# Kernel optimization log

Hardware: AMD Instinct MI355X
Metric: run time of the kernel (lower is better)

Reference implementation:

```python
import jax, jax.numpy as jnp
import numpy as np

N_QUBITS = 8
NUM_HEADS = 2
EPS = 1e-5
TWO_PI = 6.283185307179586


def _rx(state, wire, theta, n):
    # state: (B, 2**n) complex64; theta: (B,) float. PennyLane wire 0 = MSB.
    B = state.shape[0]
    st = state.reshape(B, 2 ** wire, 2, 2 ** (n - 1 - wire))
    c = jnp.cos(theta * 0.5).astype(state.dtype)[:, None, None]
    s = ((-1j) * jnp.sin(theta * 0.5).astype(state.dtype))[:, None, None]
    a0 = st[:, :, 0, :]
    a1 = st[:, :, 1, :]
    return jnp.stack([c * a0 + s * a1, s * a0 + c * a1], axis=2).reshape(B, -1)


def _cnot(state, ctrl, tgt, n):
    B = state.shape[0]
    st = state.reshape((B,) + (2,) * n)
    ax_c = ctrl + 1
    ax_t = tgt + 1
    s0 = jnp.take(st, 0, axis=ax_c)
    s1 = jnp.take(st, 1, axis=ax_c)
    ft = ax_t - 1 if ax_t > ax_c else ax_t
    s1 = jnp.flip(s1, axis=ft)
    return jnp.stack([s0, s1], axis=ax_c).reshape(B, -1)


def _vqc(x, weights):
    # AngleEmbedding (RX) + BasicEntanglerLayers (RX per wire + CNOT ring) -> <Z_i>.
    # x: (B, n) angles; weights: (L, n). Returns (B, n) real expvals.
    B, n = x.shape
    state = jnp.zeros((B, 2 ** n), dtype=jnp.complex64).at[:, 0].set(1.0)
    for w in range(n):
        state = _rx(state, w, x[:, w], n)
    pairs = [(i, (i + 1) % n) for i in range(n)] if n > 2 else ([(0, 1)] if n == 2 else [])
    for l in range(weights.shape[0]):
        for w in range(n):
            state = _rx(state, w, jnp.broadcast_to(weights[l, w], (B,)), n)
        for cw, tw in pairs:
            state = _cnot(state, cw, tw, n)
    probs = (state.real ** 2 + state.imag ** 2).reshape((B,) + (2,) * n)
    zs = []
    for w in range(n):
        axes = tuple(a for a in range(1, n + 1) if a != w + 1)
        p = jnp.sum(probs, axis=axes)  # (B, 2)
        zs.append(p[:, 0] - p[:, 1])
    return jnp.stack(zs, axis=-1)


def _layernorm(x, g, b):
    m = jnp.mean(x, axis=-1, keepdims=True)
    v = jnp.mean((x - m) ** 2, axis=-1, keepdims=True)
    return (x - m) / jnp.sqrt(v + EPS) * g + b


def setup_inputs() -> dict:
    key = jax.random.key(0)
    ks = jax.random.split(key, 10)
    E = N_QUBITS
    x = jax.random.normal(ks[0], (64, 256, E), dtype=jnp.float32)
    # TorchLayer default init: uniform(0, 2*pi)
    Wq = jax.random.uniform(ks[1], (1, E), dtype=jnp.float32) * TWO_PI
    Wk = jax.random.uniform(ks[2], (1, E), dtype=jnp.float32) * TWO_PI
    Wv = jax.random.uniform(ks[3], (1, E), dtype=jnp.float32) * TWO_PI
    Wc = jax.random.uniform(ks[4], (1, E), dtype=jnp.float32) * TWO_PI
    Wf = jax.random.uniform(ks[5], (1, E), dtype=jnp.float32) * TWO_PI
    w1 = jax.random.normal(ks[6], (E, E), dtype=jnp.float32) * 0.3
    b1 = jax.random.normal(ks[7], (E,), dtype=jnp.float32) * 0.05
    w2 = jax.random.normal(ks[8], (E, E), dtype=jnp.float32) * 0.3
    b2 = jax.random.normal(ks[9], (E,), dtype=jnp.float32) * 0.05
    gamma1 = jnp.ones((E,), dtype=jnp.float32)
    beta1 = jnp.zeros((E,), dtype=jnp.float32)
    gamma2 = jnp.ones((E,), dtype=jnp.float32)
    beta2 = jnp.zeros((E,), dtype=jnp.float32)
    return {"x": x, "Wq": Wq, "Wk": Wk, "Wv": Wv, "Wc": Wc, "Wf": Wf,
            "w1": w1, "b1": b1, "w2": w2, "b2": b2,
            "gamma1": gamma1, "beta1": beta1, "gamma2": gamma2, "beta2": beta2}


def reference(x, Wq, Wk, Wv, Wc, Wf, w1, b1, w2, b2, gamma1, beta1, gamma2, beta2):
    B, S, E = x.shape
    H = NUM_HEADS
    dk = E // H
    tok = x.reshape(B * S, E)
    Q = _vqc(tok, Wq).reshape(B, S, E)
    K = _vqc(tok, Wk).reshape(B, S, E)
    V = _vqc(tok, Wv).reshape(B, S, E)
    split = lambda t: t.reshape(B, S, H, dk).transpose(0, 2, 1, 3)
    scores = jnp.einsum('bhqd,bhkd->bhqk', split(Q), split(K)) / jnp.sqrt(jnp.float32(dk))
    attn = jax.nn.softmax(scores, axis=-1)  # dropout = identity in eval
    ctx = jnp.einsum('bhqk,bhkd->bhqd', attn, split(V)).transpose(0, 2, 1, 3).reshape(B, S, E)
    attn_out = _vqc(ctx.reshape(B * S, E), Wc).reshape(B, S, E)
    x = _layernorm(x + attn_out, gamma1, beta1)
    h = x @ w1.T + b1                       # linear1 (no activation in FeedForwardQuantum)
    hq = _vqc(h.reshape(B * S, -1), Wf).reshape(B, S, -1)
    ff = hq @ w2.T + b2                     # linear2
    x = _layernorm(x + ff, gamma2, beta2)
    return x
```

## Files before the change

kernel.cpp:

```cpp
#include <hip/hip_runtime.h>


#define SEQ 256
#define EMB 8
#define QG  64
#define NSPLIT 4

static __device__ __forceinline__ void load8f(const float* __restrict__ p, float v[8]) {
    float4 a = *reinterpret_cast<const float4*>(p);
    float4 b = *reinterpret_cast<const float4*>(p + 4);
    v[0] = a.x; v[1] = a.y; v[2] = a.z; v[3] = a.w;
    v[4] = b.x; v[5] = b.y; v[6] = b.z; v[7] = b.w;
}

static __device__ __forceinline__ void store8f(float* __restrict__ p, const float v[8]) {
    *reinterpret_cast<float4*>(p)     = make_float4(v[0], v[1], v[2], v[3]);
    *reinterpret_cast<float4*>(p + 4) = make_float4(v[4], v[5], v[6], v[7]);
}

static __device__ __forceinline__ void vqc8(const float in[8], const float W[8], float z[8]) {
    float c[8];
#pragma unroll
    for (int i = 0; i < 8; ++i) c[i] = __cosf(in[i] + W[i]);
    float t = c[1];
#pragma unroll
    for (int i = 2; i < 8; ++i) t *= c[i];
    z[0] = t;
    float acc = c[0];
#pragma unroll
    for (int i = 1; i < 8; ++i) { acc *= c[i]; z[i] = acc; }
}

static __device__ __forceinline__ void ln8(const float r[8], const float g[8], const float be[8], float o[8]) {
    float m = 0.f;
#pragma unroll
    for (int i = 0; i < 8; ++i) m += r[i];
    m *= 0.125f;
    float var = 0.f;
#pragma unroll
    for (int i = 0; i < 8; ++i) { float d = r[i] - m; var += d * d; }
    var *= 0.125f;
    float inv = rsqrtf(var + 1e-5f);
#pragma unroll
    for (int i = 0; i < 8; ++i) o[i] = (r[i] - m) * inv * g[i] + be[i];
}

__global__ __launch_bounds__(512) void vitq_kernel(
    const float* __restrict__ x,
    const float* __restrict__ Wq, const float* __restrict__ Wk,
    const float* __restrict__ Wv, const float* __restrict__ Wc,
    const float* __restrict__ Wf,
    const float* __restrict__ w1, const float* __restrict__ b1,
    const float* __restrict__ w2, const float* __restrict__ b2,
    const float* __restrict__ g1, const float* __restrict__ be1,
    const float* __restrict__ g2, const float* __restrict__ be2,
    float* __restrict__ out)
{
    __shared__ float Ks[SEQ][EMB];
    __shared__ float Vs[SEQ][EMB];
    __shared__ float P[NSPLIT][2 * QG][5];

    const int bi  = blockIdx.x;
    const int b   = bi >> 2;
    const int g   = bi & 3;
    const int tid = threadIdx.x;
    const int p   = tid & 127;
    const int j   = tid >> 7;
    const int sl  = p & 63;
    const int h   = p >> 6;
    const int s   = g * QG + sl;

    const float* xb = x + ((size_t)b * SEQ) * EMB;

    float xq[8], wrow[8], q[8];
    load8f(xb + (size_t)s * EMB, xq);
    load8f(Wq, wrow);
    vqc8(xq, wrow, q);

    {
        const int t = tid & 255;
        float xs[8], kv[8];
        load8f(xb + (size_t)t * EMB, xs);
        if (tid < 256) {
            load8f(Wk, wrow);
            vqc8(xs, wrow, kv);
            store8f(&Ks[t][0], kv);
        } else {
            load8f(Wv, wrow);
            vqc8(xs, wrow, kv);
            store8f(&Vs[t][0], kv);
        }
    }
    __syncthreads();

    const int ho = 4 * h;
    float qh[4];
#pragma unroll
    for (int d = 0; d < 4; ++d) qh[d] = q[ho + d] * 0.5f;

    float l = 0.f, acc0 = 0.f, acc1 = 0.f, acc2 = 0.f, acc3 = 0.f;
    const int k0 = j * 64;
#pragma unroll 8
    for (int kk = k0; kk < k0 + 64; ++kk) {
        float4 kr = *reinterpret_cast<const float4*>(&Ks[kk][ho]);
        float4 vr = *reinterpret_cast<const float4*>(&Vs[kk][ho]);
        float sc = qh[0] * kr.x + qh[1] * kr.y + qh[2] * kr.z + qh[3] * kr.w;
        float e  = __expf(sc);
        l    += e;
        acc0 += e * vr.x;
        acc1 += e * vr.y;
        acc2 += e * vr.z;
        acc3 += e * vr.w;
    }
    P[j][p][0] = l;
    P[j][p][1] = acc0;
    P[j][p][2] = acc1;
    P[j][p][3] = acc2;
    P[j][p][4] = acc3;
    __syncthreads();

    if (tid < QG) {
        float ctx[8];
#pragma unroll
        for (int hh = 0; hh < 2; ++hh) {
            const int pp = hh * QG + tid;
            float ll = 0.f, a0 = 0.f, a1 = 0.f, a2 = 0.f, a3 = 0.f;
#pragma unroll
            for (int jj = 0; jj < NSPLIT; ++jj) {
                ll += P[jj][pp][0];
                a0 += P[jj][pp][1];
                a1 += P[jj][pp][2];
                a2 += P[jj][pp][3];
                a3 += P[jj][pp][4];
            }
            float inv = 1.f / ll;
            ctx[4 * hh + 0] = a0 * inv;
            ctx[4 * hh + 1] = a1 * inv;
            ctx[4 * hh + 2] = a2 * inv;
            ctx[4 * hh + 3] = a3 * inv;
        }

        float ao[8];
        load8f(Wc, wrow);
        vqc8(ctx, wrow, ao);

        float r[8];
#pragma unroll
        for (int i = 0; i < 8; ++i) r[i] = xq[i] + ao[i];

        float gg[8], be[8], x1[8];
        load8f(g1, gg); load8f(be1, be);
        ln8(r, gg, be, x1);

        float wf[64], bias[8];
#pragma unroll
        for (int i = 0; i < 64; ++i) wf[i] = w1[i];
        load8f(b1, bias);
        float hv[8];
#pragma unroll
        for (int jj = 0; jj < 8; ++jj) {
            float a = bias[jj];
#pragma unroll
            for (int i = 0; i < 8; ++i) a += x1[i] * wf[jj * 8 + i];
            hv[jj] = a;
        }

        float hq[8];
        load8f(Wf, wrow);
        vqc8(hv, wrow, hq);

#pragma unroll
        for (int i = 0; i < 64; ++i) wf[i] = w2[i];
        load8f(b2, bias);
        float r2[8];
#pragma unroll
        for (int jj = 0; jj < 8; ++jj) {
            float a = bias[jj];
#pragma unroll
            for (int i = 0; i < 8; ++i) a += hq[i] * wf[jj * 8 + i];
            r2[jj] = x1[jj] + a;
        }

        float o[8];
        load8f(g2, gg); load8f(be2, be);
        ln8(r2, gg, be, o);

        store8f(out + ((size_t)(b * SEQ + s)) * EMB, o);
    }
}

extern "C" void kernel_launch(void* const* d_in, const int* in_sizes, int n_in,
                              void* d_out, int out_size, void* d_ws, size_t ws_size,
                              hipStream_t stream) {
    const float* x   = (const float*)d_in[0];
    const float* Wq  = (const float*)d_in[1];
    const float* Wk  = (const float*)d_in[2];
    const float* Wv  = (const float*)d_in[3];
    const float* Wc  = (const float*)d_in[4];
    const float* Wf  = (const float*)d_in[5];
    const float* w1  = (const float*)d_in[6];
    const float* b1  = (const float*)d_in[7];
    const float* w2  = (const float*)d_in[8];
    const float* b2  = (const float*)d_in[9];
    const float* g1  = (const float*)d_in[10];
    const float* be1 = (const float*)d_in[11];
    const float* g2  = (const float*)d_in[12];
    const float* be2 = (const float*)d_in[13];
    float* out = (float*)d_out;

    const int B = in_sizes[0] / (SEQ * EMB);
    vitq_kernel<<<B * 4, 512, 0, stream>>>(x, Wq, Wk, Wv, Wc, Wf, w1, b1, w2, b2,
                                           g1, be1, g2, be2, out);
}
```

Measured before the change: 86.93 us.

## Register-block four queries per thread and split keys sixteen ways

Each thread now computes Q for four query rows of one head and walks a 16-key slice, so every K/V row read from shared memory is reused across four queries instead of one. The key dimension is split across 16 thread groups, which means more partial results to reduce in shared memory at the end, and the per-thread register footprint grows. The query input row is reloaded later for the residual.

```diff
diff --git a/kernel.cpp b/kernel.cpp
--- a/kernel.cpp
+++ b/kernel.cpp
@@ -4,7 +4,8 @@
 #define SEQ 256
 #define EMB 8
 #define QG  64
-#define NSPLIT 4
+#define NSPLIT 16
+#define KS  16
 
 static __device__ __forceinline__ void load8f(const float* __restrict__ p, float v[8]) {
     float4 a = *reinterpret_cast<const float4*>(p);
@@ -56,26 +57,20 @@
     const float* __restrict__ g2, const float* __restrict__ be2,
     float* __restrict__ out)
 {
-    __shared__ float Ks[SEQ][EMB];
-    __shared__ float Vs[SEQ][EMB];
-    __shared__ float P[NSPLIT][2 * QG][5];
+    __shared__ float K2[SEQ][2][4];
+    __shared__ float V2[SEQ][2][4];
+    __shared__ float P[NSPLIT][2][QG][5];
 
     const int bi  = blockIdx.x;
     const int b   = bi >> 2;
     const int g   = bi & 3;
     const int tid = threadIdx.x;
-    const int p   = tid & 127;
-    const int j   = tid >> 7;
-    const int sl  = p & 63;
-    const int h   = p >> 6;
-    const int s   = g * QG + sl;
+    const int qq  = tid & 15;
+    const int h   = (tid >> 4) & 1;
+    const int j   = tid >> 5;
 
     const float* xb = x + ((size_t)b * SEQ) * EMB;
-
-    float xq[8], wrow[8], q[8];
-    load8f(xb + (size_t)s * EMB, xq);
-    load8f(Wq, wrow);
-    vqc8(xq, wrow, q);
+    float wrow[8];
 
     {
         const int t = tid & 255;
@@ -84,61 +79,75 @@
         if (tid < 256) {
             load8f(Wk, wrow);
             vqc8(xs, wrow, kv);
-            store8f(&Ks[t][0], kv);
+            store8f(&K2[t][0][0], kv);
         } else {
             load8f(Wv, wrow);
             vqc8(xs, wrow, kv);
-            store8f(&Vs[t][0], kv);
-        }
+            store8f(&V2[t][0][0], kv);
+        }
+    }
+
+    float qh[4][4];
+    load8f(Wq, wrow);
+#pragma unroll
+    for (int m = 0; m < 4; ++m) {
+        const int s = g * QG + 4 * qq + m;
+        float xq[8], q[8];
+        load8f(xb + (size_t)s * EMB, xq);
+        vqc8(xq, wrow, q);
+#pragma unroll
+        for (int d = 0; d < 4; ++d) qh[m][d] = q[4 * h + d] * 0.5f;
     }
     __syncthreads();
 
-    const int ho = 4 * h;
-    float qh[4];
-#pragma unroll
-    for (int d = 0; d < 4; ++d) qh[d] = q[ho + d] * 0.5f;
-
-    float l = 0.f, acc0 = 0.f, acc1 = 0.f, acc2 = 0.f, acc3 = 0.f;
-    const int k0 = j * 64;
-#pragma unroll 8
-    for (int kk = k0; kk < k0 + 64; ++kk) {
-        float4 kr = *reinterpret_cast<const float4*>(&Ks[kk][ho]);
-        float4 vr = *reinterpret_cast<const float4*>(&Vs[kk][ho]);
-        float sc = qh[0] * kr.x + qh[1] * kr.y + qh[2] * kr.z + qh[3] * kr.w;
-        float e  = __expf(sc);
-        l    += e;
-        acc0 += e * vr.x;
-        acc1 += e * vr.y;
-        acc2 += e * vr.z;
-        acc3 += e * vr.w;
-    }
-    P[j][p][0] = l;
-    P[j][p][1] = acc0;
-    P[j][p][2] = acc1;
-    P[j][p][3] = acc2;
-    P[j][p][4] = acc3;
+    float l[4] = {0.f, 0.f, 0.f, 0.f};
+    float a0[4] = {0.f, 0.f, 0.f, 0.f};
+    float a1[4] = {0.f, 0.f, 0.f, 0.f};
+    float a2[4] = {0.f, 0.f, 0.f, 0.f};
+    float a3[4] = {0.f, 0.f, 0.f, 0.f};
+#pragma unroll 4
+    for (int i = 0; i < KS; ++i) {
+        const int kk = j * KS + i;
+        float4 kr = *reinterpret_cast<const float4*>(&K2[kk][h][0]);
+        float4 vr = *reinterpret_cast<const float4*>(&V2[kk][h][0]);
+#pragma unroll
+        for (int m = 0; m < 4; ++m) {
+            float sc = qh[m][0] * kr.x + qh[m][1] * kr.y + qh[m][2] * kr.z + qh[m][3] * kr.w;
+            float e  = __expf(sc);
+            l[m]  += e;
+            a0[m] += e * vr.x;
+            a1[m] += e * vr.y;
+            a2[m] += e * vr.z;
+            a3[m] += e * vr.w;
+        }
+    }
+#pragma unroll
+    for (int m = 0; m < 4; ++m) {
+        float* pp = &P[j][h][4 * qq + m][0];
+        pp[0] = l[m]; pp[1] = a0[m]; pp[2] = a1[m]; pp[3] = a2[m]; pp[4] = a3[m];
+    }
     __syncthreads();
 
     if (tid < QG) {
+        const int s = g * QG + tid;
         float ctx[8];
 #pragma unroll
         for (int hh = 0; hh < 2; ++hh) {
-            const int pp = hh * QG + tid;
-            float ll = 0.f, a0 = 0.f, a1 = 0.f, a2 = 0.f, a3 = 0.f;
+            float ll = 0.f, c0 = 0.f, c1 = 0.f, c2 = 0.f, c3 = 0.f;
 #pragma unroll
             for (int jj = 0; jj < NSPLIT; ++jj) {
-                ll += P[jj][pp][0];
-                a0 += P[jj][pp][1];
-                a1 += P[jj][pp][2];
-                a2 += P[jj][pp][3];
-                a3 += P[jj][pp][4];
+                const float* pp = &P[jj][hh][tid][0];
+                ll += pp[0]; c0 += pp[1]; c1 += pp[2]; c2 += pp[3]; c3 += pp[4];
             }
             float inv = 1.f / ll;
-            ctx[4 * hh + 0] = a0 * inv;
-            ctx[4 * hh + 1] = a1 * inv;
-            ctx[4 * hh + 2] = a2 * inv;
-            ctx[4 * hh + 3] = a3 * inv;
-        }
+            ctx[4 * hh + 0] = c0 * inv;
+            ctx[4 * hh + 1] = c1 * inv;
+            ctx[4 * hh + 2] = c2 * inv;
+            ctx[4 * hh + 3] = c3 * inv;
+        }
+
+        float xq[8];
+        load8f(xb + (size_t)s * EMB, xq);
 
         float ao[8];
         load8f(Wc, wrow);
```

Measured after the change: 87.47 us. No clear change (+0.6%).
